# Kernel tuning notes

Measured on AMD Instinct MI355X. Metric: run time of the kernel, lower is better.

## Reference

```python
import jax, jax.numpy as jnp
import numpy as np

N, E, G = 50000, 1600000, 64
N_SPECIES, D_ATTR, D, N_RBF = 16, 16, 32, 8
CUTOFF = 5.0
SCALE, SHIFT = 1.0, 0.0


def setup_inputs() -> dict:
    key = jax.random.key(0)
    ks = jax.random.split(key, 20)

    def w(k, shape):
        fan_in = shape[-2] if len(shape) > 1 else shape[-1]
        return jax.random.normal(k, shape, dtype=jnp.float32) / np.sqrt(fan_in)

    return {
        "x": jax.random.randint(ks[0], (N, 1), 0, N_SPECIES),
        "pos": 3.0 * jax.random.normal(ks[1], (N, 3), dtype=jnp.float32),
        "edge_index": jax.random.randint(ks[2], (2, E), 0, N),
        "period_vec": 0.1 * jax.random.normal(ks[3], (E, 3), dtype=jnp.float32),
        "batch": jnp.sort(jax.random.randint(ks[4], (N,), 0, G)),
        "W_elem": w(ks[5], (N_SPECIES, D_ATTR)),
        "W0": w(ks[6], (D_ATTR, D)),
        "b0": jnp.zeros((D,), jnp.float32),
        "Wr1": w(ks[7], (3, N_RBF, D)),
        "br1": jnp.zeros((3, D), jnp.float32),
        "Wr2": w(ks[8], (3, D, D)),
        "Wmsg": w(ks[9], (3, D, D)),
        "Wattr": w(ks[10], (3, D_ATTR, D)),
        "Wself": w(ks[11], (3, D, D)),
        "bconv": jnp.zeros((3, D), jnp.float32),
        "wsh": w(ks[12], (3, 4)),
        "Wp1": w(ks[13], (D, 16)),
        "bp1": jnp.zeros((16,), jnp.float32),
        "Wp2": w(ks[14], (16, 1)),
        "bp2": jnp.zeros((1,), jnp.float32),
    }


def reference(x, pos, edge_index, period_vec, batch, W_elem, W0, b0, Wr1, br1,
              Wr2, Wmsg, Wattr, Wself, bconv, wsh, Wp1, bp1, Wp2, bp2):
    src, dst = edge_index[0], edge_index[1]

    # node_attr_layer: species embedding (gather), then first_atom_embed linear
    x_attr = W_elem[x[:, 0]]                              # [N, D_ATTR]
    h = x_attr @ W0 + b0                                  # [N, D]

    # edge_attr_layer: PBC edge vectors, lengths, l<=1 spherical harmonics
    edge_vec = pos[dst] - pos[src] + period_vec           # [E, 3]
    edge_len = jnp.linalg.norm(edge_vec, axis=-1, keepdims=True)  # [E, 1]
    unit = edge_vec / (edge_len + 1e-9)
    edge_sh = jnp.concatenate([jnp.ones_like(edge_len), unit], axis=-1)  # [E, 4]

    # edge_embedding_layer: Gaussian radial basis of edge lengths
    centers = jnp.linspace(0.0, CUTOFF, N_RBF, dtype=pos.dtype)
    gamma = jnp.asarray((N_RBF / CUTOFF) ** 2, pos.dtype)
    rbf = jnp.exp(-gamma * (edge_len - centers) ** 2)     # [E, N_RBF]

    # 3 conv layers: gather -> per-edge transform -> scatter-sum -> node update
    for i in range(3):
        rw = jax.nn.relu(rbf @ Wr1[i] + br1[i]) @ Wr2[i]  # [E, D] radial MLP
        sh_w = edge_sh @ wsh[i]                           # [E] sh mixing
        msg = (h[src] @ Wmsg[i]) * rw * sh_w[:, None]     # [E, D]
        agg = jax.ops.segment_sum(msg, dst, num_segments=N)  # [N, D]
        h = jax.nn.silu(agg + x_attr @ Wattr[i] + h @ Wself[i] + bconv[i])

    # post_conv layers
    h = jax.nn.silu(h @ Wp1 + bp1)                        # [N, 16]
    h = (h @ Wp2 + bp2)[:, 0]                             # [N] (squeeze)

    # scatter-sum pooling over graphs + affine energy scaling
    e = jax.ops.segment_sum(h, batch, num_segments=G)     # [G]
    return (e * SCALE + SHIFT)[:, None]                   # [G, 1]
```

## Files before the change

### kernel.cpp

```cpp
#include <hip/hip_runtime.h>
#include <hip/hip_fp16.h>
#include <math.h>

constexpr int N_NODES  = 50000;
constexpr int N_EDGES  = 1600000;
constexpr int G_GRAPHS = 64;
constexpr int D        = 32;
constexpr int D_ATTR   = 16;
constexpr int N_RBF    = 8;

constexpr int   TBL      = 8192;
constexpr int   TBL_ROWS = TBL + 1;
constexpr float LMAX     = 10.0f;

constexpr int BUCKET = 80;

constexpr int NT     = 64;
constexpr int NTILES = (N_NODES + NT - 1) / NT;
constexpr int TCAP   = 2432;
constexpr int EPB      = 2048;
constexpr int STHREADS = 512;
constexpr int EPV      = EPB / STHREADS;
constexpr int NBLK1    = (N_EDGES + EPB - 1) / EPB;

constexpr int NSLOT = NTILES * NT * BUCKET;
constexpr int TSLOT = NT * BUCKET;

constexpr int INIT_BLKS  = (N_NODES * 32 + 511) / 512;
constexpr int TABLE_BLKS = (3 * TBL_ROWS + 511) / 512;
constexpr int PREP_BLKS  = NBLK1 + INIT_BLKS + TABLE_BLKS;

typedef unsigned int  uint4v  __attribute__((ext_vector_type(4)));
typedef unsigned int  uint2v  __attribute__((ext_vector_type(2)));

__device__ __forceinline__ float silu(float x) {
    return x / (1.0f + __expf(-x));
}
__device__ __forceinline__ float h2f_bits(unsigned short u) {
    return __half2float(__ushort_as_half(u));
}
__device__ __forceinline__ __half2 h2u(unsigned v) {
    union { unsigned u; __half2 h; } c; c.u = v; return c.h;
}

__device__ __forceinline__ void accum8(uint4v t, uint4v m, float sw, float (&acc)[8]) {
    float2 p0 = __half22float2(__hmul2(h2u(t.x), h2u(m.x)));
    float2 p1 = __half22float2(__hmul2(h2u(t.y), h2u(m.y)));
    float2 p2 = __half22float2(__hmul2(h2u(t.z), h2u(m.z)));
    float2 p3 = __half22float2(__hmul2(h2u(t.w), h2u(m.w)));
    acc[0] = fmaf(p0.x, sw, acc[0]); acc[1] = fmaf(p0.y, sw, acc[1]);
    acc[2] = fmaf(p1.x, sw, acc[2]); acc[3] = fmaf(p1.y, sw, acc[3]);
    acc[4] = fmaf(p2.x, sw, acc[4]); acc[5] = fmaf(p2.y, sw, acc[5]);
    acc[6] = fmaf(p3.x, sw, acc[6]); acc[7] = fmaf(p3.y, sw, acc[7]);
}

__global__ __launch_bounds__(512, 8) void prep_kernel(const int* __restrict__ eidx,
                                                   int* __restrict__ blk_hist,
                                                   const int* __restrict__ x,
                                                   const float* __restrict__ W_elem,
                                                   const float* __restrict__ W0,
                                                   const float* __restrict__ b0,
                                                   const float* __restrict__ Wmsg0,
                                                   const float* __restrict__ Wself0,
                                                   const float* __restrict__ Wattr,
                                                   const float* __restrict__ bconv,
                                                   __half* __restrict__ hm0,
                                                   float* __restrict__ hs0,
                                                   float* __restrict__ xa1,
                                                   float* __restrict__ xa2,
                                                   float* __restrict__ out,
                                                   const float* __restrict__ Wr1,
                                                   const float* __restrict__ br1,
                                                   const float* __restrict__ Wr2,
                                                   __half* __restrict__ table) {
    __shared__ int hist[NTILES];
    int tid = threadIdx.x;
    int blk = blockIdx.x;

    if (blk < NBLK1) {
        int e0 = blk * EPB;
        for (int i = tid; i < NTILES; i += STHREADS) hist[i] = 0;
        __syncthreads();
#pragma unroll
        for (int i = 0; i < EPV; ++i) {
            int e = e0 + tid + STHREADS * i;
            if (e < N_EDGES) atomicAdd(&hist[eidx[N_EDGES + e] >> 6], 1);
        }
        __syncthreads();
        int* dst = blk_hist + (size_t)blk * NTILES;
        for (int t = tid; t < NTILES; t += STHREADS) dst[t] = hist[t];
        return;
    }
    if (blk < NBLK1 + INIT_BLKS) {
        int t = (blk - NBLK1) * 512 + tid;
        if (t < G_GRAPHS) out[t] = 0.0f;
        int n = t >> 5, c = t & 31;
        if (n >= N_NODES) return;
        int sp = x[n];
        const float* we = W_elem + sp * D_ATTR;
        float xv = (c < D_ATTR) ? we[c] : 0.0f;
        float acc = b0[c];
#pragma unroll
        for (int a = 0; a < D_ATTR; ++a) acc += we[a] * W0[a * D + c];
        float m = 0.0f, s = 0.0f;
#pragma unroll
        for (int j = 0; j < D; ++j) {
            float hj = __shfl(acc, j, 32);
            m = fmaf(hj, Wmsg0[j * D + c], m);
            s = fmaf(hj, Wself0[j * D + c], s);
        }
        float a0 = bconv[0 * D + c], a1 = bconv[1 * D + c], a2 = bconv[2 * D + c];
#pragma unroll
        for (int j = 0; j < D_ATTR; ++j) {
            float xj = __shfl(xv, j, 32);
            a0 = fmaf(xj, Wattr[0 * D_ATTR * D + j * D + c], a0);
            a1 = fmaf(xj, Wattr[1 * D_ATTR * D + j * D + c], a1);
            a2 = fmaf(xj, Wattr[2 * D_ATTR * D + j * D + c], a2);
        }
        hm0[n * D + c] = __float2half(m);
        hs0[n * D + c] = s + a0;
        xa1[n * D + c] = a1;
        xa2[n * D + c] = a2;
        return;
    }
    {
        int t = (blk - NBLK1 - INIT_BLKS) * 512 + tid;
        if (t >= 3 * TBL_ROWS) return;
        int l = t / TBL_ROWS;
        int idx = t % TBL_ROWS;
        float len = (float)idx * (LMAX / (float)TBL);
        const float gamma = (8.0f / 5.0f) * (8.0f / 5.0f);
        float rbf[N_RBF];
#pragma unroll
        for (int k = 0; k < N_RBF; ++k) {
            float dd = len - (float)k * (5.0f / 7.0f);
            rbf[k] = __expf(-gamma * dd * dd);
        }
        float outv[D];
#pragma unroll
        for (int c = 0; c < D; ++c) outv[c] = 0.0f;
        for (int j = 0; j < D; ++j) {
            float z = br1[l * D + j];
#pragma unroll
            for (int k = 0; k < N_RBF; ++k) z += rbf[k] * Wr1[l * N_RBF * D + k * D + j];
            z = fmaxf(z, 0.0f);
            const float* w2 = Wr2 + l * D * D + j * D;
#pragma unroll
            for (int c = 0; c < D; ++c) outv[c] += z * w2[c];
        }
        __half* dst = table + ((size_t)(l * TBL_ROWS + idx)) * D;
#pragma unroll
        for (int c = 0; c < D; ++c) dst[c] = __float2half(outv[c]);
    }
}

__global__ void scan_kernel(const int* __restrict__ blk_hist,
                            int* __restrict__ blk_base,
                            int* __restrict__ tile_total) {
    int t = blockIdx.x;
    int lane = threadIdx.x;
    int run = 0;
    for (int b0 = 0; b0 < NBLK1; b0 += 64) {
        int b = b0 + lane;
        int v = (b < NBLK1) ? blk_hist[(size_t)b * NTILES + t] : 0;
        int pre = v;
#pragma unroll
        for (int o = 1; o < 64; o <<= 1) {
            int w = __shfl_up(pre, o);
            if (lane >= o) pre += w;
        }
        int excl = pre - v;
        if (b < NBLK1) blk_base[(size_t)b * NTILES + t] = run + excl;
        run += __shfl(pre, 63);
    }
    if (lane == 0) tile_total[t] = run;
}

__global__ __launch_bounds__(STHREADS) void scatter_kernel(const int* __restrict__ eidx,
                                                           const float* __restrict__ pos,
                                                           const float* __restrict__ period,
                                                           const float* __restrict__ wsh,
                                                           const int* __restrict__ blk_base,
                                                           uint4v* __restrict__ bins) {
    __shared__ int hist[NTILES];
    __shared__ int basev[NTILES];
    int tid = threadIdx.x;
    int e0 = blockIdx.x * EPB;
    const int* bb = blk_base + (size_t)blockIdx.x * NTILES;
    for (int i = tid; i < NTILES; i += STHREADS) {
        hist[i] = 0;
        basev[i] = bb[i];
    }
    __syncthreads();

    int   sarr[EPV], darr[EPV];
    float vx[EPV], vy[EPV], vz[EPV];
#pragma unroll
    for (int i = 0; i < EPV; ++i) {
        int e  = e0 + tid + STHREADS * i;
        int ec = (e < N_EDGES) ? e : (N_EDGES - 1);
        int s = eidx[ec];
        int d = eidx[N_EDGES + ec];
        sarr[i] = s;
        darr[i] = d;
        vx[i] = pos[d * 3 + 0] - pos[s * 3 + 0] + period[ec * 3 + 0];
        vy[i] = pos[d * 3 + 1] - pos[s * 3 + 1] + period[ec * 3 + 1];
        vz[i] = pos[d * 3 + 2] - pos[s * 3 + 2] + period[ec * 3 + 2];
    }
    asm volatile("" ::
        "v"(vx[0]), "v"(vx[1]), "v"(vx[2]), "v"(vx[3]),
        "v"(vy[0]), "v"(vy[1]), "v"(vy[2]), "v"(vy[3]),
        "v"(vz[0]), "v"(vz[1]), "v"(vz[2]), "v"(vz[3]),
        "v"(sarr[0]), "v"(sarr[1]), "v"(sarr[2]), "v"(sarr[3]),
        "v"(darr[0]), "v"(darr[1]), "v"(darr[2]), "v"(darr[3]));
#pragma unroll
    for (int i = 0; i < EPV; ++i) {
        int e = e0 + tid + STHREADS * i;
        if (e >= N_EDGES) continue;
        float len = sqrtf(vx[i] * vx[i] + vy[i] * vy[i] + vz[i] * vz[i]);
        float inv = 1.0f / (len + 1e-9f);
        int idx = (int)fminf(len * ((float)TBL / LMAX) + 0.5f, (float)TBL);
        float sw[3];
#pragma unroll
        for (int l = 0; l < 3; ++l)
            sw[l] = wsh[l * 4 + 0] +
                    (vx[i] * wsh[l * 4 + 1] + vy[i] * wsh[l * 4 + 2] + vz[i] * wsh[l * 4 + 3]) * inv;
        int tile = darr[i] >> 6;
        int rank = atomicAdd(&hist[tile], 1);
        int slot = basev[tile] + rank;
        if (slot < TCAP) {
            unsigned u0 = (unsigned)__half_as_ushort(__float2half(sw[0]));
            unsigned u1 = (unsigned)__half_as_ushort(__float2half(sw[1]));
            unsigned u2 = (unsigned)__half_as_ushort(__float2half(sw[2]));
            uint4v r;
            r.x = (unsigned)sarr[i] | ((unsigned)idx << 16);
            r.y = (unsigned)(darr[i] & (NT - 1));
            r.z = u0 | (u1 << 16);
            r.w = u2;
            bins[(size_t)tile * TCAP + slot] = r;
        }
    }
}

__global__ __launch_bounds__(512) void shuffle_kernel(const uint4v* __restrict__ bins,
                                                      const int* __restrict__ tile_total,
                                                      unsigned int* __restrict__ xs,
                                                      unsigned short* __restrict__ swp,
                                                      int* __restrict__ count) {
    __shared__ int lcur[NT];
    __shared__ unsigned sxs[TSLOT];
    __shared__ unsigned short ssw[3][TSLOT];
    int tile = blockIdx.x;
    int tid = threadIdx.x;
    if (tid < NT) lcur[tid] = 0;
    __syncthreads();
    int cnt = tile_total[tile];
    if (cnt > TCAP) cnt = TCAP;
    const uint4v* base = bins + (size_t)tile * TCAP;
    for (int i = tid; i < cnt; i += 512) {
        uint4v r = __builtin_nontemporal_load(base + i);
        int dl = (int)(r.y & 63u);
        int slot = atomicAdd(&lcur[dl], 1);
        if (slot < BUCKET) {
            int g = dl * BUCKET + slot;
            sxs[g] = r.x;
            ssw[0][g] = (unsigned short)(r.z & 0xFFFFu);
            ssw[1][g] = (unsigned short)(r.z >> 16);
            ssw[2][g] = (unsigned short)(r.w & 0xFFFFu);
        }
    }
    __syncthreads();
    size_t gbase = (size_t)tile * TSLOT;
    {
        const uint4v* s4 = (const uint4v*)sxs;
        uint4v* g4 = (uint4v*)(xs + gbase);
        for (int i = tid; i < TSLOT / 4; i += 512) g4[i] = s4[i];
    }
#pragma unroll
    for (int l = 0; l < 3; ++l) {
        const uint4v* s4 = (const uint4v*)ssw[l];
        uint4v* g4 = (uint4v*)(swp + (size_t)l * NSLOT + gbase);
        for (int i = tid; i < TSLOT / 8; i += 512) g4[i] = s4[i];
    }
    if (tid < NT) {
        int node = tile * NT + tid;
        if (node < N_NODES) {
            int c = lcur[tid];
            count[node] = c < BUCKET ? c : BUCKET;
        }
    }
}

template <int LAYER, bool NEXT>
__global__ __launch_bounds__(256, 8) void conv_kernel(const __half* __restrict__ hm,
                            const float* __restrict__ hs,
                            const unsigned int* __restrict__ xs,
                            const unsigned short* __restrict__ swp,
                            const int* __restrict__ count,
                            const __half* __restrict__ table,
                            const float* __restrict__ Wmsg_next,
                            const float* __restrict__ Wself_next,
                            const float* __restrict__ xa_next,
                            __half* __restrict__ hm_out,
                            float* __restrict__ hs_out,
                            float* __restrict__ h_final) {
    __shared__ float sagg[4][2][32];
    int wid = (blockIdx.x * blockDim.x + threadIdx.x) >> 6;
    int na = wid * 2;
    if (na >= N_NODES) return;
    int nb = na + 1;
    int lane = threadIdx.x & 63;
    int w  = (threadIdx.x >> 6) & 3;
    int rg = lane >> 2;
    int cg = lane & 3;

    const uint4v* tab4 = (const uint4v*)(table + (size_t)LAYER * TBL_ROWS * D);
    const uint4v* hm4  = (const uint4v*)hm;
    const unsigned short* swb = swp + (size_t)LAYER * NSLOT;

    int cnta = count[na], cntb = count[nb];
    int bega = na * BUCKET, begb = nb * BUCKET;
    int mx = cnta > cntb ? cnta : cntb;

    float acca[8], accb[8];
#pragma unroll
    for (int j = 0; j < 8; ++j) { acca[j] = 0.0f; accb[j] = 0.0f; }

    for (int k = 0; k < BUCKET; k += 32) {
        int r0 = k + rg, r1 = k + 16 + rg;
        bool va0 = r0 < cnta, va1 = r1 < cnta;
        bool vb0 = r0 < cntb, vb1 = r1 < cntb;
        unsigned ua0 = va0 ? xs[bega + r0] : 0u;
        unsigned ua1 = va1 ? xs[bega + r1] : 0u;
        unsigned ub0 = vb0 ? xs[begb + r0] : 0u;
        unsigned ub1 = vb1 ? xs[begb + r1] : 0u;
        float sa0 = va0 ? h2f_bits(swb[bega + r0]) : 0.0f;
        float sa1 = va1 ? h2f_bits(swb[bega + r1]) : 0.0f;
        float sb0 = vb0 ? h2f_bits(swb[begb + r0]) : 0.0f;
        float sb1 = vb1 ? h2f_bits(swb[begb + r1]) : 0.0f;
        uint4v ta0 = tab4[(size_t)(ua0 >> 16) * 4 + cg];
        uint4v ma0 = hm4[(size_t)(ua0 & 0xFFFFu) * 4 + cg];
        uint4v ta1 = tab4[(size_t)(ua1 >> 16) * 4 + cg];
        uint4v ma1 = hm4[(size_t)(ua1 & 0xFFFFu) * 4 + cg];
        uint4v tb0 = tab4[(size_t)(ub0 >> 16) * 4 + cg];
        uint4v mb0 = hm4[(size_t)(ub0 & 0xFFFFu) * 4 + cg];
        uint4v tb1 = tab4[(size_t)(ub1 >> 16) * 4 + cg];
        uint4v mb1 = hm4[(size_t)(ub1 & 0xFFFFu) * 4 + cg];
        asm volatile("" :: "v"(ta0.x), "v"(ma0.x), "v"(ta1.x), "v"(ma1.x),
                           "v"(tb0.x), "v"(mb0.x), "v"(tb1.x), "v"(mb1.x));
        accum8(ta0, ma0, sa0, acca);
        accum8(ta1, ma1, sa1, acca);
        accum8(tb0, mb0, sb0, accb);
        accum8(tb1, mb1, sb1, accb);
        if (k + 32 >= mx) break;
    }

#pragma unroll
    for (int j = 0; j < 8; ++j) {
        acca[j] += __shfl_xor(acca[j], 4);
        acca[j] += __shfl_xor(acca[j], 8);
        acca[j] += __shfl_xor(acca[j], 16);
        acca[j] += __shfl_xor(acca[j], 32);
        accb[j] += __shfl_xor(accb[j], 4);
        accb[j] += __shfl_xor(accb[j], 8);
        accb[j] += __shfl_xor(accb[j], 16);
        accb[j] += __shfl_xor(accb[j], 32);
    }
    if (rg == 0) {
#pragma unroll
        for (int j = 0; j < 8; ++j) {
            sagg[w][0][cg * 8 + j] = acca[j];
            sagg[w][1][cg * 8 + j] = accb[j];
        }
    }
    __syncthreads();

    int c = lane & 31;
    int hi = lane >> 5;
    int mynode = hi ? nb : na;
    float agg = sagg[w][hi][c];

    float hn = silu(agg + hs[mynode * D + c]);
    if (NEXT) {
        float m = 0.0f, s2 = 0.0f;
#pragma unroll
        for (int j = 0; j < D; ++j) {
            float hj = __shfl(hn, j, 32);
            m  = fmaf(hj, Wmsg_next[j * D + c], m);
            s2 = fmaf(hj, Wself_next[j * D + c], s2);
        }
        hm_out[mynode * D + c] = __float2half(m);
        hs_out[mynode * D + c] = s2 + xa_next[mynode * D + c];
    } else {
        h_final[mynode * D + c] = hn;
    }
}

__global__ void readout_kernel(const float* __restrict__ h,
                               const int* __restrict__ batch,
                               const float* __restrict__ Wp1,
                               const float* __restrict__ bp1,
                               const float* __restrict__ Wp2,
                               const float* __restrict__ bp2,
                               float* __restrict__ out) {
    int n = blockIdx.x * blockDim.x + threadIdx.x;
    float s = 0.0f;
    int b = -1;
    if (n < N_NODES) {
        b = batch[n];
        const float* hrow = h + n * D;
        float acc2 = bp2[0];
#pragma unroll
        for (int m = 0; m < 16; ++m) {
            float a = bp1[m];
#pragma unroll
            for (int j = 0; j < D; ++j) a += hrow[j] * Wp1[j * 16 + m];
            acc2 += silu(a) * Wp2[m];
        }
        s = acc2;
    }
    unsigned long long valid = __ballot(n < N_NODES);
    if (valid == 0ull) return;
    int firstLane = __ffsll(valid) - 1;
    int b0v = __shfl(b, firstLane);
    bool ok = (b == b0v) || (n >= N_NODES);
    if (__all(ok)) {
#pragma unroll
        for (int o = 32; o > 0; o >>= 1) s += __shfl_down(s, o);
        if ((threadIdx.x & 63) == 0) atomicAdd(out + b0v, s);
    } else {
        if (n < N_NODES) atomicAdd(out + b, s);
    }
}

extern "C" void kernel_launch(void* const* d_in, const int* in_sizes, int n_in,
                              void* d_out, int out_size, void* d_ws, size_t ws_size,
                              hipStream_t stream) {
    const int*   x      = (const int*)d_in[0];
    const float* pos    = (const float*)d_in[1];
    const int*   eidx   = (const int*)d_in[2];
    const float* period = (const float*)d_in[3];
    const int*   batch  = (const int*)d_in[4];
    const float* W_elem = (const float*)d_in[5];
    const float* W0     = (const float*)d_in[6];
    const float* b0     = (const float*)d_in[7];
    const float* Wr1    = (const float*)d_in[8];
    const float* br1    = (const float*)d_in[9];
    const float* Wr2    = (const float*)d_in[10];
    const float* Wmsg   = (const float*)d_in[11];
    const float* Wattr  = (const float*)d_in[12];
    const float* Wself  = (const float*)d_in[13];
    const float* bconv  = (const float*)d_in[14];
    const float* wsh    = (const float*)d_in[15];
    const float* Wp1    = (const float*)d_in[16];
    const float* bp1    = (const float*)d_in[17];
    const float* Wp2    = (const float*)d_in[18];
    const float* bp2    = (const float*)d_in[19];

    char* base = (char*)d_ws;
    size_t off = 0;
    auto carve = [&](size_t bytes) -> void* {
        void* p = base + off;
        off = (off + bytes + 255) & ~(size_t)255;
        return p;
    };
    __half*         hm_a        = (__half*)carve((size_t)N_NODES * D * 2);
    __half*         hm_b        = (__half*)carve((size_t)N_NODES * D * 2);
    float*          hs_a        = (float*)carve((size_t)N_NODES * D * 4);
    float*          hs_b        = (float*)carve((size_t)N_NODES * D * 4);
    float*          xa1         = (float*)carve((size_t)N_NODES * D * 4);
    float*          xa2         = (float*)carve((size_t)N_NODES * D * 4);
    float*          h_final     = (float*)carve((size_t)N_NODES * D * 4);
    unsigned int*   xs          = (unsigned int*)carve((size_t)NSLOT * 4);
    unsigned short* swp         = (unsigned short*)carve((size_t)3 * NSLOT * 2);
    uint4v*         bins        = (uint4v*)carve((size_t)NTILES * TCAP * 16);
    int*            blk_hist    = (int*)carve((size_t)NBLK1 * NTILES * 4);
    int*            blk_base    = (int*)carve((size_t)NBLK1 * NTILES * 4);
    int*            tile_total  = (int*)carve((size_t)NTILES * 4);
    int*            count       = (int*)carve((size_t)NTILES * NT * 4);
    __half*         table       = (__half*)carve((size_t)3 * TBL_ROWS * D * 2);
    (void)ws_size; (void)in_sizes; (void)n_in; (void)out_size;

    prep_kernel<<<PREP_BLKS, 512, 0, stream>>>(
        eidx, blk_hist,
        x, W_elem, W0, b0, Wmsg + 0 * D * D, Wself + 0 * D * D, Wattr, bconv,
        hm_a, hs_a, xa1, xa2, (float*)d_out,
        Wr1, br1, Wr2, table);
    scan_kernel<<<NTILES, 64, 0, stream>>>(blk_hist, blk_base, tile_total);
    scatter_kernel<<<NBLK1, STHREADS, 0, stream>>>(eidx, pos, period, wsh, blk_base, bins);
    shuffle_kernel<<<NTILES, 512, 0, stream>>>(bins, tile_total, xs, swp, count);

    int cwaves = (N_NODES + 1) / 2;
    int cgrid  = (cwaves * 64 + 255) / 256;
    conv_kernel<0, true><<<cgrid, 256, 0, stream>>>(
        hm_a, hs_a, xs, swp, count, table, Wmsg + 1 * D * D, Wself + 1 * D * D, xa1,
        hm_b, hs_b, nullptr);
    conv_kernel<1, true><<<cgrid, 256, 0, stream>>>(
        hm_b, hs_b, xs, swp, count, table, Wmsg + 2 * D * D, Wself + 2 * D * D, xa2,
        hm_a, hs_a, nullptr);
    conv_kernel<2, false><<<cgrid, 256, 0, stream>>>(
        hm_a, hs_a, xs, swp, count, table, nullptr, nullptr, nullptr,
        nullptr, nullptr, h_final);

    readout_kernel<<<(N_NODES + 255) / 256, 256, 0, stream>>>(h_final, batch, Wp1, bp1, Wp2, bp2,
                                                              (float*)d_out);
}
```

Measured before the change: 361.1 us.

## Replace histogram+scan binning with per-block atomic cursor reservation in scatter

Removes the per-block histogram pass in prep and the separate scan kernel. The scatter kernel now builds its local tile histogram itself and reserves output ranges through global atomicAdd on per-tile cursors, which prep_kernel zeroes. Block size doubles to 1024 threads and 4096 edges per block. This saves a kernel launch, the blk_hist and blk_base traffic, and a second read of the dst indices in a separate kernel. In exchange, the order of edges within each tile becomes nondeterministic, and contention on the global atomics rises.

```diff
diff --git a/kernel.cpp b/kernel.cpp
--- a/kernel.cpp
+++ b/kernel.cpp
@@ -18,8 +18,8 @@
 constexpr int NT     = 64;
 constexpr int NTILES = (N_NODES + NT - 1) / NT;
 constexpr int TCAP   = 2432;
-constexpr int EPB      = 2048;
-constexpr int STHREADS = 512;
+constexpr int EPB      = 4096;
+constexpr int STHREADS = 1024;
 constexpr int EPV      = EPB / STHREADS;
 constexpr int NBLK1    = (N_EDGES + EPB - 1) / EPB;
 
@@ -28,7 +28,7 @@
 
 constexpr int INIT_BLKS  = (N_NODES * 32 + 511) / 512;
 constexpr int TABLE_BLKS = (3 * TBL_ROWS + 511) / 512;
-constexpr int PREP_BLKS  = NBLK1 + INIT_BLKS + TABLE_BLKS;
+constexpr int PREP_BLKS  = INIT_BLKS + TABLE_BLKS;
 
 typedef unsigned int  uint4v  __attribute__((ext_vector_type(4)));
 typedef unsigned int  uint2v  __attribute__((ext_vector_type(2)));
@@ -54,9 +54,7 @@
     acc[6] = fmaf(p3.x, sw, acc[6]); acc[7] = fmaf(p3.y, sw, acc[7]);
 }
 
-__global__ __launch_bounds__(512, 8) void prep_kernel(const int* __restrict__ eidx,
-                                                   int* __restrict__ blk_hist,
-                                                   const int* __restrict__ x,
+__global__ __launch_bounds__(512) void prep_kernel(const int* __restrict__ x,
                                                    const float* __restrict__ W_elem,
                                                    const float* __restrict__ W0,
                                                    const float* __restrict__ b0,
@@ -68,32 +66,19 @@
                                                    float* __restrict__ hs0,
                                                    float* __restrict__ xa1,
                                                    float* __restrict__ xa2,
+                                                   int* __restrict__ tile_cursor,
                                                    float* __restrict__ out,
                                                    const float* __restrict__ Wr1,
                                                    const float* __restrict__ br1,
                                                    const float* __restrict__ Wr2,
                                                    __half* __restrict__ table) {
-    __shared__ int hist[NTILES];
     int tid = threadIdx.x;
     int blk = blockIdx.x;
 
-    if (blk < NBLK1) {
-        int e0 = blk * EPB;
-        for (int i = tid; i < NTILES; i += STHREADS) hist[i] = 0;
-        __syncthreads();
-#pragma unroll
-        for (int i = 0; i < EPV; ++i) {
-            int e = e0 + tid + STHREADS * i;
-            if (e < N_EDGES) atomicAdd(&hist[eidx[N_EDGES + e] >> 6], 1);
-        }
-        __syncthreads();
-        int* dst = blk_hist + (size_t)blk * NTILES;
-        for (int t = tid; t < NTILES; t += STHREADS) dst[t] = hist[t];
-        return;
-    }
-    if (blk < NBLK1 + INIT_BLKS) {
-        int t = (blk - NBLK1) * 512 + tid;
+    if (blk < INIT_BLKS) {
+        int t = blk * 512 + tid;
         if (t < G_GRAPHS) out[t] = 0.0f;
+        if (t < NTILES) tile_cursor[t] = 0;
         int n = t >> 5, c = t & 31;
         if (n >= N_NODES) return;
         int sp = x[n];
@@ -124,7 +109,7 @@
         return;
     }
     {
-        int t = (blk - NBLK1 - INIT_BLKS) * 512 + tid;
+        int t = (blk - INIT_BLKS) * 512 + tid;
         if (t >= 3 * TBL_ROWS) return;
         int l = t / TBL_ROWS;
         int idx = t % TBL_ROWS;
@@ -154,42 +139,28 @@
     }
 }
 
-__global__ void scan_kernel(const int* __restrict__ blk_hist,
-                            int* __restrict__ blk_base,
-                            int* __restrict__ tile_total) {
-    int t = blockIdx.x;
-    int lane = threadIdx.x;
-    int run = 0;
-    for (int b0 = 0; b0 < NBLK1; b0 += 64) {
-        int b = b0 + lane;
-        int v = (b < NBLK1) ? blk_hist[(size_t)b * NTILES + t] : 0;
-        int pre = v;
-#pragma unroll
-        for (int o = 1; o < 64; o <<= 1) {
-            int w = __shfl_up(pre, o);
-            if (lane >= o) pre += w;
-        }
-        int excl = pre - v;
-        if (b < NBLK1) blk_base[(size_t)b * NTILES + t] = run + excl;
-        run += __shfl(pre, 63);
-    }
-    if (lane == 0) tile_total[t] = run;
-}
-
-__global__ __launch_bounds__(STHREADS) void scatter_kernel(const int* __restrict__ eidx,
-                                                           const float* __restrict__ pos,
-                                                           const float* __restrict__ period,
-                                                           const float* __restrict__ wsh,
-                                                           const int* __restrict__ blk_base,
-                                                           uint4v* __restrict__ bins) {
+__global__ __launch_bounds__(STHREADS, 4) void scatter_kernel(const int* __restrict__ eidx,
+                                                              const float* __restrict__ pos,
+                                                              const float* __restrict__ period,
+                                                              const float* __restrict__ wsh,
+                                                              int* __restrict__ tile_cursor,
+                                                              uint4v* __restrict__ bins) {
     __shared__ int hist[NTILES];
     __shared__ int basev[NTILES];
     int tid = threadIdx.x;
     int e0 = blockIdx.x * EPB;
-    const int* bb = blk_base + (size_t)blockIdx.x * NTILES;
-    for (int i = tid; i < NTILES; i += STHREADS) {
-        hist[i] = 0;
-        basev[i] = bb[i];
+    for (int i = tid; i < NTILES; i += STHREADS) hist[i] = 0;
+    __syncthreads();
+#pragma unroll
+    for (int i = 0; i < EPV; ++i) {
+        int e = e0 + tid + STHREADS * i;
+        if (e < N_EDGES) atomicAdd(&hist[eidx[N_EDGES + e] >> 6], 1);
+    }
+    __syncthreads();
+    for (int t = tid; t < NTILES; t += STHREADS) {
+        int cnt = hist[t];
+        basev[t] = (cnt > 0) ? atomicAdd(&tile_cursor[t], cnt) : 0;
+        hist[t] = 0;
     }
     __syncthreads();
 
@@ -474,21 +445,18 @@
     unsigned int*   xs          = (unsigned int*)carve((size_t)NSLOT * 4);
     unsigned short* swp         = (unsigned short*)carve((size_t)3 * NSLOT * 2);
     uint4v*         bins        = (uint4v*)carve((size_t)NTILES * TCAP * 16);
-    int*            blk_hist    = (int*)carve((size_t)NBLK1 * NTILES * 4);
-    int*            blk_base    = (int*)carve((size_t)NBLK1 * NTILES * 4);
-    int*            tile_total  = (int*)carve((size_t)NTILES * 4);
+    int*            tile_cursor = (int*)carve((size_t)NTILES * 4);
     int*            count       = (int*)carve((size_t)NTILES * NT * 4);
     __half*         table       = (__half*)carve((size_t)3 * TBL_ROWS * D * 2);
     (void)ws_size; (void)in_sizes; (void)n_in; (void)out_size;
 
     prep_kernel<<<PREP_BLKS, 512, 0, stream>>>(
-        eidx, blk_hist,
         x, W_elem, W0, b0, Wmsg + 0 * D * D, Wself + 0 * D * D, Wattr, bconv,
-        hm_a, hs_a, xa1, xa2, (float*)d_out,
+        hm_a, hs_a, xa1, xa2, tile_cursor, (float*)d_out,
         Wr1, br1, Wr2, table);
-    scan_kernel<<<NTILES, 64, 0, stream>>>(blk_hist, blk_base, tile_total);
-    scatter_kernel<<<NBLK1, STHREADS, 0, stream>>>(eidx, pos, period, wsh, blk_base, bins);
-    shuffle_kernel<<<NTILES, 512, 0, stream>>>(bins, tile_total, xs, swp, count);
+    scatter_kernel<<<NBLK1, STHREADS, 0, stream>>>(eidx, pos, period, wsh,
+                                                   tile_cursor, bins);
+    shuffle_kernel<<<NTILES, 512, 0, stream>>>(bins, tile_cursor, xs, swp, count);
 
     int cwaves = (N_NODES + 1) / 2;
     int cgrid  = (cwaves * 64 + 255) / 256;
```

New measurement: 345.2 us (median of 2 runs). 4.4% less time.
